# Performance work log

Measured on AMD Instinct MI355X. Metric: run time of the kernel, lower is better.

The kernel has to match this reference:

```python
import jax, jax.numpy as jnp
import numpy as np

B, N, DIM = 2, 2048, 1024
HEADS, DH, NUM_MEM = 8, 64, 4
EPS = 1e-5


def layer_norm(x, gamma):
    mu = x.mean(-1, keepdims=True)
    var = ((x - mu) ** 2).mean(-1, keepdims=True)
    return (x - mu) * jax.lax.rsqrt(var + EPS) * gamma


def setup_inputs() -> dict:
    key = jax.random.key(0)
    ks = jax.random.split(key, 7)
    x = jax.random.normal(ks[0], (B, N, DIM), jnp.float32)
    mask = jax.random.randint(ks[1], (B, N), 0, 2) > 0
    attn_bias = jax.random.normal(ks[2], (HEADS, N, N), jnp.float32) * 0.02
    gamma = jnp.ones((DIM,), jnp.float32)
    Wq = jax.random.normal(ks[3], (DIM, HEADS * DH), jnp.float32) * (DIM ** -0.5)
    Wkv = jax.random.normal(ks[4], (DIM, 2 * DH), jnp.float32) * (DIM ** -0.5)
    mem_kv = jax.random.normal(ks[5], (2, NUM_MEM, DH), jnp.float32)
    Wout = jax.random.normal(ks[6], (HEADS * DH, DIM), jnp.float32) * ((HEADS * DH) ** -0.5)
    return dict(x=x, attn_bias=attn_bias, gamma=gamma, Wq=Wq, Wkv=Wkv,
                mem_kv=mem_kv, Wout=Wout, mask=mask)


def reference(x, attn_bias, gamma, Wq, Wkv, mem_kv, Wout, mask):
    b, n, _ = x.shape
    # norm applied to query path only; kv comes from pre-norm x (self-attention)
    xn = layer_norm(x, gamma)
    q = (xn @ Wq).reshape(b, n, HEADS, DH).transpose(0, 2, 1, 3) * (DH ** -0.5)  # b h n d
    kv = x @ Wkv  # multi-query: single shared kv head
    k, v = kv[..., :DH], kv[..., DH:]
    mk = jnp.broadcast_to(mem_kv[0], (b, NUM_MEM, DH))
    mv = jnp.broadcast_to(mem_kv[1], (b, NUM_MEM, DH))
    k = jnp.concatenate([mk, k], axis=1)  # b (m+n) d
    v = jnp.concatenate([mv, v], axis=1)
    j = n + NUM_MEM
    bias = jnp.pad(attn_bias, ((0, 0), (0, 0), (NUM_MEM, 0)))  # zero bias on mem tokens
    maskp = jnp.pad(mask, ((0, 0), (NUM_MEM, 0)), constant_values=True)
    sim = jnp.einsum('bhid,bjd->bhij', q, k) + bias
    neg = -jnp.finfo(sim.dtype).max
    sim = jnp.where(maskp[:, None, None, :], sim, neg)
    causal = jnp.triu(jnp.ones((n, j), bool), k=NUM_MEM + 1)  # mem tokens always visible
    sim = jnp.where(causal, neg, sim)
    attn = jax.nn.softmax(sim, axis=-1)
    out = jnp.einsum('bhij,bjd->bhid', attn, v)
    out = out.transpose(0, 2, 1, 3).reshape(b, n, HEADS * DH)
    return out @ Wout
```

## Files before the change

kernel.cpp:

```cpp
#include <hip/hip_runtime.h>
#include <hip/hip_bf16.h>
#include <float.h>

#define B_ 2
#define N_ 2048
#define DIM_ 1024
#define HEADS_ 8
#define DH_ 64
#define NUM_MEM_ 4
#define ROWS_ (B_ * N_)
#define QCOLS_ (HEADS_ * DH_)
#define JTOT_ (N_ + NUM_MEM_)
#define JPAD_ 2176
#define CHUNKS_PER_BH_ 77

typedef __attribute__((ext_vector_type(8))) short short8v;
typedef __attribute__((ext_vector_type(4))) float f32x4;

static __device__ __forceinline__ ushort f2b(float f) {
    __hip_bfloat16 hb = __float2bfloat16(f);
    return *(ushort*)&hb;
}
static __device__ __forceinline__ uint pk2(float a, float b) {
    return ((uint)f2b(b) << 16) | (uint)f2b(a);
}
static __device__ __forceinline__ float b2f_lo(uint u) {
    union { uint x; float f; } c; c.x = u << 16; return c.f;
}
static __device__ __forceinline__ float b2f_hi(uint u) {
    union { uint x; float f; } c; c.x = u & 0xffff0000u; return c.f;
}

__global__ __launch_bounds__(256) void ln_cast_kernel(const float* __restrict__ x,
                                                      const float* __restrict__ gamma,
                                                      ushort* __restrict__ xb,
                                                      ushort* __restrict__ xnb) {
    int row = blockIdx.x;
    const float4 v = ((const float4*)(x + (size_t)row * DIM_))[threadIdx.x];
    float s  = v.x + v.y + v.z + v.w;
    float s2 = v.x * v.x + v.y * v.y + v.z * v.z + v.w * v.w;
    #pragma unroll
    for (int off = 32; off > 0; off >>= 1) {
        s  += __shfl_down(s, off);
        s2 += __shfl_down(s2, off);
    }
    __shared__ float ws1[4], ws2[4];
    int lane = threadIdx.x & 63, wid = threadIdx.x >> 6;
    if (lane == 0) { ws1[wid] = s; ws2[wid] = s2; }
    __syncthreads();
    float tot  = ws1[0] + ws1[1] + ws1[2] + ws1[3];
    float tot2 = ws2[0] + ws2[1] + ws2[2] + ws2[3];
    float mu  = tot * (1.0f / DIM_);
    float var = tot2 * (1.0f / DIM_) - mu * mu;
    float rs  = rsqrtf(var + 1e-5f);
    const float4 g = ((const float4*)gamma)[threadIdx.x];
    float vv[4] = {v.x, v.y, v.z, v.w};
    float gg[4] = {g.x, g.y, g.z, g.w};
    ushort xo[4], xno[4];
    #pragma unroll
    for (int j = 0; j < 4; ++j) {
        xo[j]  = f2b(vv[j]);
        xno[j] = f2b((vv[j] - mu) * rs * gg[j]);
    }
    *(int2*)(xb  + (size_t)row * DIM_ + threadIdx.x * 4) = *(int2*)xo;
    *(int2*)(xnb + (size_t)row * DIM_ + threadIdx.x * 4) = *(int2*)xno;
}

static __device__ __forceinline__ void wtrans_body(const float* __restrict__ W,
                                                   ushort* __restrict__ Wt,
                                                   int K, int N, int t) {
    int n = t % N;
    int k0 = (t / N) * 8;
    ushort u[8];
    #pragma unroll
    for (int j = 0; j < 8; ++j) u[j] = f2b(W[(size_t)(k0 + j) * N + n]);
    *(int4*)(Wt + (size_t)n * K + k0) = *(int4*)u;
}

__global__ __launch_bounds__(256) void prep_kernel(const float* __restrict__ Wq,
                                                   const float* __restrict__ Wkv,
                                                   const float* __restrict__ Wout,
                                                   const float* __restrict__ mem_kv,
                                                   ushort* __restrict__ Wqt,
                                                   ushort* __restrict__ Wkvt,
                                                   ushort* __restrict__ Woutt,
                                                   ushort* __restrict__ Kb,
                                                   ushort* __restrict__ Vt) {
    int bid = blockIdx.x;
    int tid = threadIdx.x;
    if (bid < 256) {
        wtrans_body(Wq, Wqt, DIM_, QCOLS_, bid * 256 + tid);
    } else if (bid < 320) {
        wtrans_body(Wkv, Wkvt, DIM_, 2 * DH_, (bid - 256) * 256 + tid);
    } else if (bid < 576) {
        wtrans_body(Wout, Woutt, QCOLS_, DIM_, (bid - 320) * 256 + tid);
    } else {
        int t = (bid - 576) * 256 + tid;
        int d  = t & 63;
        int ji = (t >> 6) & 127;
        int b  = t >> 13;
        int j  = (ji < NUM_MEM_) ? ji : (2048 + ji);
        float kv_ = 0.f, vv = 0.f;
        if (ji < NUM_MEM_) {
            kv_ = mem_kv[ji * DH_ + d];
            vv  = mem_kv[NUM_MEM_ * DH_ + ji * DH_ + d];
        }
        Kb[((size_t)(b * JPAD_) + j) * DH_ + d] = f2b(kv_);
        Vt[((size_t)(b * DH_) + d) * JPAD_ + j] = f2b(vv);
    }
}

template<int MODE, int BM>
__global__ __launch_bounds__(256) void gemm_bf16(const ushort* __restrict__ A,
                                                 const ushort* __restrict__ Bt,
                                                 void* __restrict__ C,
                                                 void* __restrict__ C2,
                                                 int M, int N, int K) {
    constexpr int RT = BM / 64;
    __shared__ ushort As[BM][40];
    __shared__ ushort Bs[64][40];
    int tid = threadIdx.x;
    int w = tid >> 6, l = tid & 63, lg = l >> 4, ll = l & 15;
    int r0 = blockIdx.y * BM, c0 = blockIdx.x * 64;

    int arow = tid >> 2;
    int achk = (tid & 3) * 8;
    const ushort* Ap  = A + (size_t)(r0 + arow) * K + achk;
    const ushort* Ap2 = Ap + (size_t)64 * K;
    const ushort* Bp  = Bt + (size_t)(c0 + arow) * K + achk;

    int4 a0 = *(const int4*)Ap;
    int4 a1;
    if constexpr (RT == 2) a1 = *(const int4*)Ap2;
    int4 b0 = *(const int4*)Bp;

    f32x4 acc[RT][4] = {};

    int nk = K / 32;
    for (int ks = 0; ks < nk; ++ks) {
        __syncthreads();
        *(int4*)&As[arow][achk] = a0;
        if constexpr (RT == 2) *(int4*)&As[arow + 64][achk] = a1;
        *(int4*)&Bs[arow][achk] = b0;
        __syncthreads();
        int kn = (ks + 1 < nk) ? (ks + 1) * 32 : 0;
        a0 = *(const int4*)(Ap + kn);
        if constexpr (RT == 2) a1 = *(const int4*)(Ap2 + kn);
        b0 = *(const int4*)(Bp + kn);
        short8v af[RT], bf[4];
        #pragma unroll
        for (int rt = 0; rt < RT; ++rt)
            af[rt] = *(const short8v*)&As[w * 16 * RT + rt * 16 + ll][lg * 8];
        #pragma unroll
        for (int ct = 0; ct < 4; ++ct)
            bf[ct] = *(const short8v*)&Bs[ct * 16 + ll][lg * 8];
        __builtin_amdgcn_s_setprio(1);
        #pragma unroll
        for (int rt = 0; rt < RT; ++rt)
            #pragma unroll
            for (int ct = 0; ct < 4; ++ct)
                acc[rt][ct] = __builtin_amdgcn_mfma_f32_16x16x32_bf16(af[rt], bf[ct], acc[rt][ct], 0, 0, 0);
        __builtin_amdgcn_s_setprio(0);
    }

    #pragma unroll
    for (int rt = 0; rt < RT; ++rt) {
        #pragma unroll
        for (int ct = 0; ct < 4; ++ct) {
            #pragma unroll
            for (int r = 0; r < 4; ++r) {
                int row = r0 + w * 16 * RT + rt * 16 + lg * 4 + r;
                int col = c0 + ct * 16 + ll;
                float val = acc[rt][ct][r];
                if (MODE == 0) {
                    ((ushort*)C)[(size_t)row * QCOLS_ + col] = f2b(val * 0.125f);
                } else if (MODE == 1) {
                    int b = row >> 11;
                    int j = (row & 2047) + NUM_MEM_;
                    if (col < DH_)
                        ((ushort*)C)[((size_t)(b * JPAD_) + j) * DH_ + col] = f2b(val);
                    else
                        ((ushort*)C2)[((size_t)(b * DH_) + (col - DH_)) * JPAD_ + j] = f2b(val);
                } else {
                    ((float*)C)[(size_t)row * DIM_ + col] = val;
                }
            }
        }
    }
}

__global__ __launch_bounds__(256) void fattn_split_kernel(const ushort* __restrict__ qb,
                                                          const ushort* __restrict__ Kb,
                                                          const ushort* __restrict__ Vt,
                                                          const float* __restrict__ bias,
                                                          const int* __restrict__ mask,
                                                          float* __restrict__ part_O,
                                                          float* __restrict__ part_ml) {
    __shared__ ushort Ks[64][72];
    __shared__ ushort Vs[64][72];
    __shared__ ushort Pt[4][16][72];
    __shared__ ushort Bb[64][68];

    int cid = blockIdx.x;
    int bh  = cid / CHUNKS_PER_BH_;
    int rem = cid - bh * CHUNKS_PER_BH_;
    int b = bh >> 3, h = bh & 7;
    int qt = 0, ci = 0;
    {
        int cum = 0;
        #pragma unroll 1
        for (int t = 0; t < 32; ++t) {
            int c = (t + 10) / 9;
            if (rem < cum + c) { qt = t; ci = rem - cum; break; }
            cum += c;
        }
    }
    int nt = qt + 2;
    int nc = (qt + 10) / 9;
    int t0 = ci * nt / nc;
    int t1 = (ci + 1) * nt / nc;
    int q0 = qt * 64;

    int tid = threadIdx.x;
    int w  = tid >> 6;
    int l  = tid & 63;
    int lg = l >> 4;
    int ll = l & 15;
    int i_row = q0 + w * 16 + ll;

    short8v aq0, aq1;
    {
        const ushort* qp = qb + ((size_t)(b * N_ + i_row)) * QCOLS_ + h * DH_;
        aq0 = *(const short8v*)(qp + lg * 8);
        aq1 = *(const short8v*)(qp + 32 + lg * 8);
    }

    int trow = tid >> 5;
    int tpc  = tid & 31;
    const float* bias_rb = bias + ((size_t)h * N_ + q0 + trow) * N_;
    const int* mrowp = mask + b * N_;

    int sr = tid >> 3, sc = (tid & 7) * 8;
    const ushort* KbB = Kb + (size_t)b * JPAD_ * DH_;
    const ushort* VtB = Vt + (size_t)b * DH_ * JPAD_;

    auto stage_bias = [&](int j0, uint* bbx) {
        int j_e = j0 + 2 * tpc;
        int sj  = j_e - NUM_MEM_;
        int sjc = sj < 0 ? 0 : (sj > N_ - 2 ? N_ - 2 : sj);
        int2 mk2 = *(const int2*)(mrowp + sjc);
        float2 bv[8];
        #pragma unroll
        for (int p = 0; p < 8; ++p)
            bv[p] = *(const float2*)(bias_rb + (size_t)(8 * p) * N_ + sjc);
        #pragma unroll
        for (int p = 0; p < 8; ++p) {
            int i_s = q0 + trow + 8 * p;
            float v0 = (j_e     < NUM_MEM_) ? 0.f : (mk2.x ? bv[p].x : -1e30f);
            float v1 = (j_e + 1 < NUM_MEM_) ? 0.f : (mk2.y ? bv[p].y : -1e30f);
            v0 = (j_e     <= i_s + NUM_MEM_) ? v0 : -1e30f;
            v1 = (j_e + 1 <= i_s + NUM_MEM_) ? v1 : -1e30f;
            bbx[p] = pk2(v0, v1);
        }
    };

    int jp0 = t0 * 64;
    int4 kr0 = *(const int4*)(KbB + (size_t)(jp0 + sr) * DH_ + sc);
    int4 kr1 = *(const int4*)(KbB + (size_t)(jp0 + sr + 32) * DH_ + sc);
    int4 vr0 = *(const int4*)(VtB + (size_t)sr * JPAD_ + jp0 + sc);
    int4 vr1 = *(const int4*)(VtB + (size_t)(sr + 32) * JPAD_ + jp0 + sc);
    uint bbc[8], bbn[8];
    stage_bias(jp0, bbc);

    f32x4 oacc[4] = {};
    float mrow1 = -1e30f, lsum1 = 0.f;

    for (int jt = t0; jt < t1; ++jt) {
        __syncthreads();
        *(int4*)&Ks[sr][sc]      = kr0;
        *(int4*)&Ks[sr + 32][sc] = kr1;
        *(int4*)&Vs[sr][sc]      = vr0;
        *(int4*)&Vs[sr + 32][sc] = vr1;
        #pragma unroll
        for (int p = 0; p < 8; ++p)
            *(uint*)&Bb[trow + 8 * p][2 * tpc] = bbc[p];
        __syncthreads();

        int jn0 = (jt + 1 < t1 ? jt + 1 : jt) * 64;
        kr0 = *(const int4*)(KbB + (size_t)(jn0 + sr) * DH_ + sc);
        kr1 = *(const int4*)(KbB + (size_t)(jn0 + sr + 32) * DH_ + sc);
        vr0 = *(const int4*)(VtB + (size_t)sr * JPAD_ + jn0 + sc);
        vr1 = *(const int4*)(VtB + (size_t)(sr + 32) * JPAD_ + jn0 + sc);
        stage_bias(jn0, bbn);

        float s[4][4];
        #pragma unroll
        for (int ct = 0; ct < 4; ++ct) {
            f32x4 acc = {};
            short8v bk0 = *(const short8v*)&Ks[ct * 16 + ll][lg * 8];
            short8v bk1 = *(const short8v*)&Ks[ct * 16 + ll][32 + lg * 8];
            __builtin_amdgcn_s_setprio(1);
            acc = __builtin_amdgcn_mfma_f32_16x16x32_bf16(bk0, aq0, acc, 0, 0, 0);
            acc = __builtin_amdgcn_mfma_f32_16x16x32_bf16(bk1, aq1, acc, 0, 0, 0);
            __builtin_amdgcn_s_setprio(0);
            uint2 ub = *(const uint2*)&Bb[w * 16 + ll][ct * 16 + lg * 4];
            s[ct][0] = acc[0] + b2f_lo(ub.x);
            s[ct][1] = acc[1] + b2f_hi(ub.x);
            s[ct][2] = acc[2] + b2f_lo(ub.y);
            s[ct][3] = acc[3] + b2f_hi(ub.y);
        }

        float m01 = fmaxf(fmaxf(s[0][0], s[0][1]), fmaxf(s[0][2], s[0][3]));
        float m23 = fmaxf(fmaxf(s[1][0], s[1][1]), fmaxf(s[1][2], s[1][3]));
        float m45 = fmaxf(fmaxf(s[2][0], s[2][1]), fmaxf(s[2][2], s[2][3]));
        float m67 = fmaxf(fmaxf(s[3][0], s[3][1]), fmaxf(s[3][2], s[3][3]));
        float m = fmaxf(fmaxf(m01, m23), fmaxf(m45, m67));
        m = fmaxf(m, __shfl_xor(m, 16));
        m = fmaxf(m, __shfl_xor(m, 32));
        float mn = fmaxf(mrow1, m);
        float scl = __expf(mrow1 - mn);
        mrow1 = mn;

        float ps = 0.f;
        #pragma unroll
        for (int ct = 0; ct < 4; ++ct)
            #pragma unroll
            for (int r = 0; r < 4; ++r) {
                float p = __expf(s[ct][r] - mn);
                s[ct][r] = p;
                ps += p;
            }
        ps += __shfl_xor(ps, 16);
        ps += __shfl_xor(ps, 32);
        lsum1 = lsum1 * scl + ps;

        #pragma unroll
        for (int ct = 0; ct < 4; ++ct) {
            uint2 pu;
            pu.x = pk2(s[ct][0], s[ct][1]);
            pu.y = pk2(s[ct][2], s[ct][3]);
            *(uint2*)&Pt[w][ll][ct * 16 + lg * 4] = pu;
        }
        #pragma unroll
        for (int dt = 0; dt < 4; ++dt)
            #pragma unroll
            for (int r = 0; r < 4; ++r) oacc[dt][r] *= scl;

        #pragma unroll
        for (int c = 0; c < 2; ++c) {
            short8v ptf = *(const short8v*)&Pt[w][ll][c * 32 + lg * 8];
            __builtin_amdgcn_s_setprio(1);
            #pragma unroll
            for (int dt = 0; dt < 4; ++dt) {
                short8v bv = *(const short8v*)&Vs[dt * 16 + ll][c * 32 + lg * 8];
                oacc[dt] = __builtin_amdgcn_mfma_f32_16x16x32_bf16(bv, ptf, oacc[dt], 0, 0, 0);
            }
            __builtin_amdgcn_s_setprio(0);
        }

        #pragma unroll
        for (int u = 0; u < 8; ++u) bbc[u] = bbn[u];
    }

    int slot = (bh * 32 + qt) * 4 + ci;
    float* po = part_O + (size_t)slot * 4096;
    #pragma unroll
    for (int dt = 0; dt < 4; ++dt)
        *(f32x4*)&po[(w * 16 + ll) * 64 + dt * 16 + lg * 4] = oacc[dt];
    if (lg == 0) {
        part_ml[(size_t)slot * 128 + (w * 16 + ll) * 2]     = mrow1;
        part_ml[(size_t)slot * 128 + (w * 16 + ll) * 2 + 1] = lsum1;
    }
}

__global__ __launch_bounds__(256) void merge_kernel(const float* __restrict__ part_O,
                                                    const float* __restrict__ part_ml,
                                                    ushort* __restrict__ attn_ob) {
    int bid = blockIdx.x;
    int qt = bid & 31;
    int bh = bid >> 5;
    int b = bh >> 3, h = bh & 7;
    int nc = (qt + 10) / 9;
    int tid = threadIdx.x;
    int row = tid >> 2;
    int dseg = (tid & 3) * 16;
    int slot0 = bid * 4;

    float M = -1e30f;
    #pragma unroll
    for (int c = 0; c < 4; ++c) {
        if (c >= nc) break;
        M = fmaxf(M, part_ml[(size_t)(slot0 + c) * 128 + row * 2]);
    }
    float den = 0.f;
    float num[16] = {};
    #pragma unroll
    for (int c = 0; c < 4; ++c) {
        if (c >= nc) break;
        float m_c = part_ml[(size_t)(slot0 + c) * 128 + row * 2];
        float l_c = part_ml[(size_t)(slot0 + c) * 128 + row * 2 + 1];
        float wgt = __expf(m_c - M);
        den += wgt * l_c;
        const float4* src = (const float4*)(part_O + (size_t)(slot0 + c) * 4096 + row * 64 + dseg);
        #pragma unroll
        for (int e = 0; e < 4; ++e) {
            float4 v = src[e];
            num[e * 4 + 0] += wgt * v.x;
            num[e * 4 + 1] += wgt * v.y;
            num[e * 4 + 2] += wgt * v.z;
            num[e * 4 + 3] += wgt * v.w;
        }
    }
    float inv = 1.f / den;
    ushort o[16];
    #pragma unroll
    for (int e = 0; e < 16; ++e) o[e] = f2b(num[e] * inv);
    int i = qt * 64 + row;
    ushort* dst = attn_ob + ((size_t)(b * N_ + i)) * QCOLS_ + h * DH_ + dseg;
    *(int4*)dst = *(int4*)o;
    *(int4*)(dst + 8) = *(int4*)(o + 8);
}

extern "C" void kernel_launch(void* const* d_in, const int* in_sizes, int n_in,
                              void* d_out, int out_size, void* d_ws, size_t ws_size,
                              hipStream_t stream) {
    const float* x         = (const float*)d_in[0];
    const float* attn_bias = (const float*)d_in[1];
    const float* gamma     = (const float*)d_in[2];
    const float* Wq        = (const float*)d_in[3];
    const float* Wkv       = (const float*)d_in[4];
    const float* mem_kv    = (const float*)d_in[5];
    const float* Wout      = (const float*)d_in[6];
    const int*   mask      = (const int*)d_in[7];
    float* out = (float*)d_out;

    char* wsb = (char*)d_ws;
    ushort* xb      = (ushort*)wsb;
    ushort* xnb     = (ushort*)(wsb + (8u  << 20));
    ushort* qb      = (ushort*)(wsb + (16u << 20));
    ushort* attn_ob = (ushort*)(wsb + (20u << 20));
    ushort* Kb      = (ushort*)(wsb + (24u << 20));
    ushort* Vt      = (ushort*)(wsb + (25u << 20));
    ushort* Wqt     = (ushort*)(wsb + (26u << 20));
    ushort* Wkvt    = (ushort*)(wsb + (27u << 20));
    ushort* Woutt   = (ushort*)(wsb + (28u << 20));
    float*  part_O  = (float*)(wsb + (32u << 20));
    float*  part_ml = (float*)(wsb + (64u << 20));

    ln_cast_kernel<<<ROWS_, 256, 0, stream>>>(x, gamma, xb, xnb);
    prep_kernel<<<640, 256, 0, stream>>>(Wq, Wkv, Wout, mem_kv, Wqt, Wkvt, Woutt, Kb, Vt);

    gemm_bf16<0, 64><<<dim3(QCOLS_ / 64, ROWS_ / 64), 256, 0, stream>>>(xnb, Wqt, qb, nullptr, ROWS_, QCOLS_, DIM_);
    gemm_bf16<1, 64><<<dim3((2 * DH_) / 64, ROWS_ / 64), 256, 0, stream>>>(xb, Wkvt, Kb, Vt, ROWS_, 2 * DH_, DIM_);
    fattn_split_kernel<<<16 * CHUNKS_PER_BH_, 256, 0, stream>>>(qb, Kb, Vt, attn_bias, mask, part_O, part_ml);
    merge_kernel<<<512, 256, 0, stream>>>(part_O, part_ml, attn_ob);
    gemm_bf16<2, 128><<<dim3(DIM_ / 64, ROWS_ / 128), 256, 0, stream>>>(attn_ob, Woutt, out, nullptr, ROWS_, DIM_, QCOLS_);
}
```

Baseline: 110.5 us.

## Load attention bias directly into MFMA layout and precompute additive key mask

Drops the LDS staging of the bias tile. Each lane now loads its own float4 of bias straight from global memory in the MFMA output layout, and adds a precomputed bf16 additive key mask built in prep_kernel. Causal masking is applied arithmetically only on the diagonal tiles, and the kernel gets launch_bounds occupancy hint 4. This saves LDS traffic, a shared buffer and per-tile packing work, but gives up the register prefetch of the next tile's bias, so bias loads now sit on the critical path. Bias is also added at full fp32 precision instead of bf16.

```diff
diff --git a/kernel.cpp b/kernel.cpp
--- a/kernel.cpp
+++ b/kernel.cpp
@@ -81,11 +81,13 @@
                                                    const float* __restrict__ Wkv,
                                                    const float* __restrict__ Wout,
                                                    const float* __restrict__ mem_kv,
+                                                   const int* __restrict__ mask,
                                                    ushort* __restrict__ Wqt,
                                                    ushort* __restrict__ Wkvt,
                                                    ushort* __restrict__ Woutt,
                                                    ushort* __restrict__ Kb,
-                                                   ushort* __restrict__ Vt) {
+                                                   ushort* __restrict__ Vt,
+                                                   ushort* __restrict__ amask) {
     int bid = blockIdx.x;
     int tid = threadIdx.x;
     if (bid < 256) {
@@ -94,7 +96,7 @@
         wtrans_body(Wkv, Wkvt, DIM_, 2 * DH_, (bid - 256) * 256 + tid);
     } else if (bid < 576) {
         wtrans_body(Wout, Woutt, QCOLS_, DIM_, (bid - 320) * 256 + tid);
-    } else {
+    } else if (bid < 640) {
         int t = (bid - 576) * 256 + tid;
         int d  = t & 63;
         int ji = (t >> 6) & 127;
@@ -107,6 +109,17 @@
         }
         Kb[((size_t)(b * JPAD_) + j) * DH_ + d] = f2b(kv_);
         Vt[((size_t)(b * DH_) + d) * JPAD_ + j] = f2b(vv);
+    } else {
+        int t = (bid - 640) * 256 + tid;
+        if (t < B_ * JPAD_) {
+            int b = t / JPAD_;
+            int j = t % JPAD_;
+            float v;
+            if (j < NUM_MEM_) v = 0.f;
+            else if (j < JTOT_) v = mask[b * N_ + (j - NUM_MEM_)] ? 0.f : -1e30f;
+            else v = -1e30f;
+            amask[(size_t)b * JPAD_ + j] = f2b(v);
+        }
     }
 }
 
@@ -189,17 +202,16 @@
     }
 }
 
-__global__ __launch_bounds__(256) void fattn_split_kernel(const ushort* __restrict__ qb,
-                                                          const ushort* __restrict__ Kb,
-                                                          const ushort* __restrict__ Vt,
-                                                          const float* __restrict__ bias,
-                                                          const int* __restrict__ mask,
-                                                          float* __restrict__ part_O,
-                                                          float* __restrict__ part_ml) {
+__global__ __launch_bounds__(256, 4) void fattn_split_kernel(const ushort* __restrict__ qb,
+                                                             const ushort* __restrict__ Kb,
+                                                             const ushort* __restrict__ Vt,
+                                                             const float* __restrict__ bias,
+                                                             const ushort* __restrict__ amask,
+                                                             float* __restrict__ part_O,
+                                                             float* __restrict__ part_ml) {
     __shared__ ushort Ks[64][72];
     __shared__ ushort Vs[64][72];
     __shared__ ushort Pt[4][16][72];
-    __shared__ ushort Bb[64][68];
 
     int cid = blockIdx.x;
     int bh  = cid / CHUNKS_PER_BH_;
@@ -235,63 +247,47 @@
         aq1 = *(const short8v*)(qp + 32 + lg * 8);
     }
 
-    int trow = tid >> 5;
-    int tpc  = tid & 31;
-    const float* bias_rb = bias + ((size_t)h * N_ + q0 + trow) * N_;
-    const int* mrowp = mask + b * N_;
+    const float*  bias_row = bias + ((size_t)h * N_ + i_row) * N_;
+    const ushort* am_row   = amask + (size_t)b * JPAD_;
 
     int sr = tid >> 3, sc = (tid & 7) * 8;
     const ushort* KbB = Kb + (size_t)b * JPAD_ * DH_;
     const ushort* VtB = Vt + (size_t)b * DH_ * JPAD_;
-
-    auto stage_bias = [&](int j0, uint* bbx) {
-        int j_e = j0 + 2 * tpc;
-        int sj  = j_e - NUM_MEM_;
-        int sjc = sj < 0 ? 0 : (sj > N_ - 2 ? N_ - 2 : sj);
-        int2 mk2 = *(const int2*)(mrowp + sjc);
-        float2 bv[8];
-        #pragma unroll
-        for (int p = 0; p < 8; ++p)
-            bv[p] = *(const float2*)(bias_rb + (size_t)(8 * p) * N_ + sjc);
-        #pragma unroll
-        for (int p = 0; p < 8; ++p) {
-            int i_s = q0 + trow + 8 * p;
-            float v0 = (j_e     < NUM_MEM_) ? 0.f : (mk2.x ? bv[p].x : -1e30f);
-            float v1 = (j_e + 1 < NUM_MEM_) ? 0.f : (mk2.y ? bv[p].y : -1e30f);
-            v0 = (j_e     <= i_s + NUM_MEM_) ? v0 : -1e30f;
-            v1 = (j_e + 1 <= i_s + NUM_MEM_) ? v1 : -1e30f;
-            bbx[p] = pk2(v0, v1);
-        }
-    };
 
     int jp0 = t0 * 64;
     int4 kr0 = *(const int4*)(KbB + (size_t)(jp0 + sr) * DH_ + sc);
     int4 kr1 = *(const int4*)(KbB + (size_t)(jp0 + sr + 32) * DH_ + sc);
     int4 vr0 = *(const int4*)(VtB + (size_t)sr * JPAD_ + jp0 + sc);
     int4 vr1 = *(const int4*)(VtB + (size_t)(sr + 32) * JPAD_ + jp0 + sc);
-    uint bbc[8], bbn[8];
-    stage_bias(jp0, bbc);
 
     f32x4 oacc[4] = {};
     float mrow1 = -1e30f, lsum1 = 0.f;
 
     for (int jt = t0; jt < t1; ++jt) {
+        int j0 = jt * 64;
         __syncthreads();
         *(int4*)&Ks[sr][sc]      = kr0;
         *(int4*)&Ks[sr + 32][sc] = kr1;
         *(int4*)&Vs[sr][sc]      = vr0;
         *(int4*)&Vs[sr + 32][sc] = vr1;
-        #pragma unroll
-        for (int p = 0; p < 8; ++p)
-            *(uint*)&Bb[trow + 8 * p][2 * tpc] = bbc[p];
         __syncthreads();
+
+        float4 bb[4];
+        uint2  am[4];
+        #pragma unroll
+        for (int ct = 0; ct < 4; ++ct) {
+            int js = j0 + ct * 16 + lg * 4;
+            int sj = js - NUM_MEM_;
+            int sjc = sj < 0 ? 0 : (sj > N_ - 4 ? N_ - 4 : sj);
+            bb[ct] = *(const float4*)(bias_row + sjc);
+            am[ct] = *(const uint2*)(am_row + js);
+        }
 
         int jn0 = (jt + 1 < t1 ? jt + 1 : jt) * 64;
         kr0 = *(const int4*)(KbB + (size_t)(jn0 + sr) * DH_ + sc);
         kr1 = *(const int4*)(KbB + (size_t)(jn0 + sr + 32) * DH_ + sc);
         vr0 = *(const int4*)(VtB + (size_t)sr * JPAD_ + jn0 + sc);
         vr1 = *(const int4*)(VtB + (size_t)(sr + 32) * JPAD_ + jn0 + sc);
-        stage_bias(jn0, bbn);
 
         float s[4][4];
         #pragma unroll
@@ -303,11 +299,25 @@
             acc = __builtin_amdgcn_mfma_f32_16x16x32_bf16(bk0, aq0, acc, 0, 0, 0);
             acc = __builtin_amdgcn_mfma_f32_16x16x32_bf16(bk1, aq1, acc, 0, 0, 0);
             __builtin_amdgcn_s_setprio(0);
-            uint2 ub = *(const uint2*)&Bb[w * 16 + ll][ct * 16 + lg * 4];
-            s[ct][0] = acc[0] + b2f_lo(ub.x);
-            s[ct][1] = acc[1] + b2f_hi(ub.x);
-            s[ct][2] = acc[2] + b2f_lo(ub.y);
-            s[ct][3] = acc[3] + b2f_hi(ub.y);
+            float amf[4] = { b2f_lo(am[ct].x), b2f_hi(am[ct].x),
+                             b2f_lo(am[ct].y), b2f_hi(am[ct].y) };
+            #pragma unroll
+            for (int r = 0; r < 4; ++r)
+                s[ct][r] = acc[r] + bb[ct][r] + amf[r];
+            if (ct == 0 && jt == 0) {
+                #pragma unroll
+                for (int r = 0; r < 4; ++r)
+                    if (lg == 0) s[0][r] = acc[r];
+            }
+        }
+        if (jt >= qt) {
+            #pragma unroll
+            for (int ct = 0; ct < 4; ++ct)
+                #pragma unroll
+                for (int r = 0; r < 4; ++r) {
+                    int js = j0 + ct * 16 + lg * 4 + r;
+                    s[ct][r] = (js <= i_row + NUM_MEM_) ? s[ct][r] : -1e30f;
+                }
         }
 
         float m01 = fmaxf(fmaxf(s[0][0], s[0][1]), fmaxf(s[0][2], s[0][3]));
@@ -357,9 +367,6 @@
             }
             __builtin_amdgcn_s_setprio(0);
         }
-
-        #pragma unroll
-        for (int u = 0; u < 8; ++u) bbc[u] = bbn[u];
     }
 
     int slot = (bh * 32 + qt) * 4 + ci;
@@ -444,15 +451,16 @@
     ushort* Wqt     = (ushort*)(wsb + (26u << 20));
     ushort* Wkvt    = (ushort*)(wsb + (27u << 20));
     ushort* Woutt   = (ushort*)(wsb + (28u << 20));
+    ushort* amask   = (ushort*)(wsb + (29u << 20));
     float*  part_O  = (float*)(wsb + (32u << 20));
     float*  part_ml = (float*)(wsb + (64u << 20));
 
     ln_cast_kernel<<<ROWS_, 256, 0, stream>>>(x, gamma, xb, xnb);
-    prep_kernel<<<640, 256, 0, stream>>>(Wq, Wkv, Wout, mem_kv, Wqt, Wkvt, Woutt, Kb, Vt);
+    prep_kernel<<<657, 256, 0, stream>>>(Wq, Wkv, Wout, mem_kv, mask, Wqt, Wkvt, Woutt, Kb, Vt, amask);
 
     gemm_bf16<0, 64><<<dim3(QCOLS_ / 64, ROWS_ / 64), 256, 0, stream>>>(xnb, Wqt, qb, nullptr, ROWS_, QCOLS_, DIM_);
     gemm_bf16<1, 64><<<dim3((2 * DH_) / 64, ROWS_ / 64), 256, 0, stream>>>(xb, Wkvt, Kb, Vt, ROWS_, 2 * DH_, DIM_);
-    fattn_split_kernel<<<16 * CHUNKS_PER_BH_, 256, 0, stream>>>(qb, Kb, Vt, attn_bias, mask, part_O, part_ml);
+    fattn_split_kernel<<<16 * CHUNKS_PER_BH_, 256, 0, stream>>>(qb, Kb, Vt, attn_bias, amask, part_O, part_ml);
     merge_kernel<<<512, 256, 0, stream>>>(part_O, part_ml, attn_ob);
     gemm_bf16<2, 128><<<dim3(DIM_ / 64, ROWS_ / 128), 256, 0, stream>>>(attn_ob, Woutt, out, nullptr, ROWS_, DIM_, QCOLS_);
 }
```

Result: faster. 108.2 us (-2.1%).

## Precompute additive bf16 mask, defer bias folding, store bf16 partials, cap occupancy

Applied to the files above, without the earlier changes.

Adds a prep pass that converts the boolean key mask into an additive bf16 row (0 or -1e30) per batch. The attention kernel then reads one packed uint instead of an int2, and folds bias plus mask after the compute phase instead of right after the prefetch, which shortens the live range of the staged bias registers. Split-K partial outputs are written as bf16 instead of fp32, halving partial-output traffic between the attention and merge kernels at some precision cost. It also sets launch_bounds min-blocks to 4 and leaves an unused fold_bias lambda in place.

```diff
diff --git a/kernel.cpp b/kernel.cpp
--- a/kernel.cpp
+++ b/kernel.cpp
@@ -81,11 +81,13 @@
                                                    const float* __restrict__ Wkv,
                                                    const float* __restrict__ Wout,
                                                    const float* __restrict__ mem_kv,
+                                                   const int* __restrict__ mask,
                                                    ushort* __restrict__ Wqt,
                                                    ushort* __restrict__ Wkvt,
                                                    ushort* __restrict__ Woutt,
                                                    ushort* __restrict__ Kb,
-                                                   ushort* __restrict__ Vt) {
+                                                   ushort* __restrict__ Vt,
+                                                   ushort* __restrict__ amask) {
     int bid = blockIdx.x;
     int tid = threadIdx.x;
     if (bid < 256) {
@@ -94,7 +96,7 @@
         wtrans_body(Wkv, Wkvt, DIM_, 2 * DH_, (bid - 256) * 256 + tid);
     } else if (bid < 576) {
         wtrans_body(Wout, Woutt, QCOLS_, DIM_, (bid - 320) * 256 + tid);
-    } else {
+    } else if (bid < 640) {
         int t = (bid - 576) * 256 + tid;
         int d  = t & 63;
         int ji = (t >> 6) & 127;
@@ -107,6 +109,17 @@
         }
         Kb[((size_t)(b * JPAD_) + j) * DH_ + d] = f2b(kv_);
         Vt[((size_t)(b * DH_) + d) * JPAD_ + j] = f2b(vv);
+    } else {
+        int t = (bid - 640) * 256 + tid;
+        if (t < B_ * JPAD_) {
+            int b = t / JPAD_;
+            int j = t % JPAD_;
+            float v;
+            if (j < NUM_MEM_) v = 0.f;
+            else if (j < JTOT_) v = mask[b * N_ + (j - NUM_MEM_)] ? 0.f : -1e30f;
+            else v = -1e30f;
+            amask[(size_t)b * JPAD_ + j] = f2b(v);
+        }
     }
 }
 
@@ -189,13 +202,13 @@
     }
 }
 
-__global__ __launch_bounds__(256) void fattn_split_kernel(const ushort* __restrict__ qb,
-                                                          const ushort* __restrict__ Kb,
-                                                          const ushort* __restrict__ Vt,
-                                                          const float* __restrict__ bias,
-                                                          const int* __restrict__ mask,
-                                                          float* __restrict__ part_O,
-                                                          float* __restrict__ part_ml) {
+__global__ __launch_bounds__(256, 4) void fattn_split_kernel(const ushort* __restrict__ qb,
+                                                             const ushort* __restrict__ Kb,
+                                                             const ushort* __restrict__ Vt,
+                                                             const float* __restrict__ bias,
+                                                             const ushort* __restrict__ amask,
+                                                             ushort* __restrict__ part_O,
+                                                             float* __restrict__ part_ml) {
     __shared__ ushort Ks[64][72];
     __shared__ ushort Vs[64][72];
     __shared__ ushort Pt[4][16][72];
@@ -237,40 +250,44 @@
 
     int trow = tid >> 5;
     int tpc  = tid & 31;
-    const float* bias_rb = bias + ((size_t)h * N_ + q0 + trow) * N_;
-    const int* mrowp = mask + b * N_;
+    const float*  bias_rb = bias + ((size_t)h * N_ + q0 + trow) * N_;
+    const ushort* am_row  = amask + (size_t)b * JPAD_;
 
     int sr = tid >> 3, sc = (tid & 7) * 8;
     const ushort* KbB = Kb + (size_t)b * JPAD_ * DH_;
     const ushort* VtB = Vt + (size_t)b * DH_ * JPAD_;
 
-    auto stage_bias = [&](int j0, uint* bbx) {
-        int j_e = j0 + 2 * tpc;
-        int sj  = j_e - NUM_MEM_;
-        int sjc = sj < 0 ? 0 : (sj > N_ - 2 ? N_ - 2 : sj);
-        int2 mk2 = *(const int2*)(mrowp + sjc);
-        float2 bv[8];
-        #pragma unroll
-        for (int p = 0; p < 8; ++p)
-            bv[p] = *(const float2*)(bias_rb + (size_t)(8 * p) * N_ + sjc);
-        #pragma unroll
-        for (int p = 0; p < 8; ++p) {
-            int i_s = q0 + trow + 8 * p;
-            float v0 = (j_e     < NUM_MEM_) ? 0.f : (mk2.x ? bv[p].x : -1e30f);
-            float v1 = (j_e + 1 < NUM_MEM_) ? 0.f : (mk2.y ? bv[p].y : -1e30f);
-            v0 = (j_e     <= i_s + NUM_MEM_) ? v0 : -1e30f;
-            v1 = (j_e + 1 <= i_s + NUM_MEM_) ? v1 : -1e30f;
-            bbx[p] = pk2(v0, v1);
-        }
+    auto fold_bias = [&](const float2* bv, uint am2, uint* bbx) {
+        float amf0 = b2f_lo(am2), amf1 = b2f_hi(am2);
+        int j_e = 0;
+        (void)j_e;
     };
+    (void)fold_bias;
 
     int jp0 = t0 * 64;
     int4 kr0 = *(const int4*)(KbB + (size_t)(jp0 + sr) * DH_ + sc);
     int4 kr1 = *(const int4*)(KbB + (size_t)(jp0 + sr + 32) * DH_ + sc);
     int4 vr0 = *(const int4*)(VtB + (size_t)sr * JPAD_ + jp0 + sc);
     int4 vr1 = *(const int4*)(VtB + (size_t)(sr + 32) * JPAD_ + jp0 + sc);
-    uint bbc[8], bbn[8];
-    stage_bias(jp0, bbc);
+
+    uint bbc[8];
+    {
+        int j_e = jp0 + 2 * tpc;
+        int sj  = j_e - NUM_MEM_;
+        int sjc = sj < 0 ? 0 : (sj > N_ - 2 ? N_ - 2 : sj);
+        uint am2 = *(const uint*)(am_row + j_e);
+        float amf0 = b2f_lo(am2), amf1 = b2f_hi(am2);
+        #pragma unroll
+        for (int p = 0; p < 8; ++p) {
+            float2 bv = *(const float2*)(bias_rb + (size_t)(8 * p) * N_ + sjc);
+            int i_s = q0 + trow + 8 * p;
+            float v0 = (j_e     < NUM_MEM_) ? 0.f : bv.x + amf0;
+            float v1 = (j_e + 1 < NUM_MEM_) ? 0.f : bv.y + amf1;
+            v0 = (j_e     <= i_s + NUM_MEM_) ? v0 : -1e30f;
+            v1 = (j_e + 1 <= i_s + NUM_MEM_) ? v1 : -1e30f;
+            bbc[p] = pk2(v0, v1);
+        }
+    }
 
     f32x4 oacc[4] = {};
     float mrow1 = -1e30f, lsum1 = 0.f;
@@ -291,7 +308,14 @@
         kr1 = *(const int4*)(KbB + (size_t)(jn0 + sr + 32) * DH_ + sc);
         vr0 = *(const int4*)(VtB + (size_t)sr * JPAD_ + jn0 + sc);
         vr1 = *(const int4*)(VtB + (size_t)(sr + 32) * JPAD_ + jn0 + sc);
-        stage_bias(jn0, bbn);
+        int j_e = jn0 + 2 * tpc;
+        int sj  = j_e - NUM_MEM_;
+        int sjc = sj < 0 ? 0 : (sj > N_ - 2 ? N_ - 2 : sj);
+        uint am2n = *(const uint*)(am_row + j_e);
+        float2 bvn[8];
+        #pragma unroll
+        for (int p = 0; p < 8; ++p)
+            bvn[p] = *(const float2*)(bias_rb + (size_t)(8 * p) * N_ + sjc);
 
         float s[4][4];
         #pragma unroll
@@ -358,22 +382,36 @@
             __builtin_amdgcn_s_setprio(0);
         }
 
-        #pragma unroll
-        for (int u = 0; u < 8; ++u) bbc[u] = bbn[u];
+        {
+            float amf0 = b2f_lo(am2n), amf1 = b2f_hi(am2n);
+            #pragma unroll
+            for (int p = 0; p < 8; ++p) {
+                int i_s = q0 + trow + 8 * p;
+                float v0 = (j_e     < NUM_MEM_) ? 0.f : bvn[p].x + amf0;
+                float v1 = (j_e + 1 < NUM_MEM_) ? 0.f : bvn[p].y + amf1;
+                v0 = (j_e     <= i_s + NUM_MEM_) ? v0 : -1e30f;
+                v1 = (j_e + 1 <= i_s + NUM_MEM_) ? v1 : -1e30f;
+                bbc[p] = pk2(v0, v1);
+            }
+        }
     }
 
     int slot = (bh * 32 + qt) * 4 + ci;
-    float* po = part_O + (size_t)slot * 4096;
-    #pragma unroll
-    for (int dt = 0; dt < 4; ++dt)
-        *(f32x4*)&po[(w * 16 + ll) * 64 + dt * 16 + lg * 4] = oacc[dt];
+    ushort* po = part_O + (size_t)slot * 4096;
+    #pragma unroll
+    for (int dt = 0; dt < 4; ++dt) {
+        uint2 pu;
+        pu.x = pk2(oacc[dt][0], oacc[dt][1]);
+        pu.y = pk2(oacc[dt][2], oacc[dt][3]);
+        *(uint2*)&po[(w * 16 + ll) * 64 + dt * 16 + lg * 4] = pu;
+    }
     if (lg == 0) {
         part_ml[(size_t)slot * 128 + (w * 16 + ll) * 2]     = mrow1;
         part_ml[(size_t)slot * 128 + (w * 16 + ll) * 2 + 1] = lsum1;
     }
 }
 
-__global__ __launch_bounds__(256) void merge_kernel(const float* __restrict__ part_O,
+__global__ __launch_bounds__(256) void merge_kernel(const ushort* __restrict__ part_O,
                                                     const float* __restrict__ part_ml,
                                                     ushort* __restrict__ attn_ob) {
     int bid = blockIdx.x;
@@ -401,14 +439,15 @@
         float l_c = part_ml[(size_t)(slot0 + c) * 128 + row * 2 + 1];
         float wgt = __expf(m_c - M);
         den += wgt * l_c;
-        const float4* src = (const float4*)(part_O + (size_t)(slot0 + c) * 4096 + row * 64 + dseg);
-        #pragma unroll
-        for (int e = 0; e < 4; ++e) {
-            float4 v = src[e];
-            num[e * 4 + 0] += wgt * v.x;
-            num[e * 4 + 1] += wgt * v.y;
-            num[e * 4 + 2] += wgt * v.z;
-            num[e * 4 + 3] += wgt * v.w;
+        const uint4* src = (const uint4*)(part_O + (size_t)(slot0 + c) * 4096 + row * 64 + dseg);
+        uint4 v0 = src[0];
+        uint uu[8] = { v0.x, v0.y, v0.z, v0.w, 0, 0, 0, 0 };
+        uint4 v1 = src[1];
+        uu[4] = v1.x; uu[5] = v1.y; uu[6] = v1.z; uu[7] = v1.w;
+        #pragma unroll
+        for (int e = 0; e < 8; ++e) {
+            num[e * 2 + 0] += wgt * b2f_lo(uu[e]);
+            num[e * 2 + 1] += wgt * b2f_hi(uu[e]);
         }
     }
     float inv = 1.f / den;
@@ -444,15 +483,16 @@
     ushort* Wqt     = (ushort*)(wsb + (26u << 20));
     ushort* Wkvt    = (ushort*)(wsb + (27u << 20));
     ushort* Woutt   = (ushort*)(wsb + (28u << 20));
-    float*  part_O  = (float*)(wsb + (32u << 20));
+    ushort* amask   = (ushort*)(wsb + (29u << 20));
+    ushort* part_O  = (ushort*)(wsb + (32u << 20));
     float*  part_ml = (float*)(wsb + (64u << 20));
 
     ln_cast_kernel<<<ROWS_, 256, 0, stream>>>(x, gamma, xb, xnb);
-    prep_kernel<<<640, 256, 0, stream>>>(Wq, Wkv, Wout, mem_kv, Wqt, Wkvt, Woutt, Kb, Vt);
+    prep_kernel<<<657, 256, 0, stream>>>(Wq, Wkv, Wout, mem_kv, mask, Wqt, Wkvt, Woutt, Kb, Vt, amask);
 
     gemm_bf16<0, 64><<<dim3(QCOLS_ / 64, ROWS_ / 64), 256, 0, stream>>>(xnb, Wqt, qb, nullptr, ROWS_, QCOLS_, DIM_);
     gemm_bf16<1, 64><<<dim3((2 * DH_) / 64, ROWS_ / 64), 256, 0, stream>>>(xb, Wkvt, Kb, Vt, ROWS_, 2 * DH_, DIM_);
-    fattn_split_kernel<<<16 * CHUNKS_PER_BH_, 256, 0, stream>>>(qb, Kb, Vt, attn_bias, mask, part_O, part_ml);
+    fattn_split_kernel<<<16 * CHUNKS_PER_BH_, 256, 0, stream>>>(qb, Kb, Vt, attn_bias, amask, part_O, part_ml);
     merge_kernel<<<512, 256, 0, stream>>>(part_O, part_ml, attn_ob);
     gemm_bf16<2, 128><<<dim3(DIM_ / 64, ROWS_ / 128), 256, 0, stream>>>(attn_ob, Woutt, out, nullptr, ROWS_, DIM_, QCOLS_);
 }
```

Measured after the change: 103.2 us. 1.07x faster.
